# Optimization experiments

Hardware: AMD Instinct MI355X
Metric: run time of the kernel (lower is better)

Reference implementation:

```python
import jax, jax.numpy as jnp
import numpy as np

# Hypernetwork config (matches init_kwargs)
INP = 4096      # inp_size
MSK = 64        # mask_size
HID = 64        # node_hidden_size (target-net hidden)
OUT = 10        # out_size (target outputs)
L1, L2, L3 = 64, 256, 128  # hypernet trunk layers
B = 16384       # batch
WVEC = MSK * HID + HID + HID * OUT + OUT  # 4810 generated weights per sample


def _linear_params(key, fan_in, fan_out):
    # torch.nn.Linear default init: U(-1/sqrt(fan_in), 1/sqrt(fan_in))
    lim = 1.0 / np.sqrt(fan_in)
    kw, kb = jax.random.split(key)
    W = jax.random.uniform(kw, (fan_out, fan_in), minval=-lim, maxval=lim, dtype=jnp.float32)
    b = jax.random.uniform(kb, (fan_out,), minval=-lim, maxval=lim, dtype=jnp.float32)
    return W, b


def setup_inputs() -> dict:
    key = jax.random.key(0)
    ks = jax.random.split(key, 6)
    W1, b1 = _linear_params(ks[0], INP, L1)
    W2, b2 = _linear_params(ks[1], L1, L2)
    W3, b3 = _linear_params(ks[2], L2, L3)
    W4, b4 = _linear_params(ks[3], L3, WVEC)
    data = jax.random.normal(ks[4], (B, INP), dtype=jnp.float32)
    mask_idx = jnp.sort(jax.random.randint(ks[5], (B, MSK), 0, INP), axis=1)  # int indices of active features
    return dict(data=data, mask_idx=mask_idx,
                W1=W1, b1=b1, W2=W2, b2=b2, W3=W3, b3=b3, W4=W4, b4=b4)


def reference(data, mask_idx, W1, b1, W2, b2, W3, b3, W4, b4):
    b = data.shape[0]
    # Rebuild the float binary mask [B, INP] from indices (scatter ones)
    rows = jnp.arange(b)[:, None]
    mask = jnp.zeros((b, INP), dtype=data.dtype).at[rows, mask_idx].set(1.0)

    # craft_network: 4-layer MLP on the mask (dropout is identity in eval / for reference)
    h = jax.nn.relu(mask @ W1.T + b1)
    h = jax.nn.relu(h @ W2.T + b2)
    h = jax.nn.relu(h @ W3.T + b3)
    w = h @ W4.T + b4  # [B, WVEC] generated weights per sample

    # Split per-sample generated weights (same layout as InsertableNet)
    iw_end = MSK * HID
    ib_end = iw_end + HID
    ow_end = ib_end + HID * OUT
    inp_w = w[:, :iw_end].reshape(b, HID, MSK)       # [B, H, M]
    inp_b = w[:, iw_end:ib_end]                      # [B, H]
    out_w = w[:, ib_end:ow_end].reshape(b, OUT, HID) # [B, O, H]
    out_b = w[:, ow_end:]                            # [B, O]

    # Per-sample gather of masked features: data[i, mask[i]] -> [B, M]
    xm = jnp.take_along_axis(data, mask_idx, axis=1)

    # Batched tiny 2-layer MLP (replaces the per-sample Python loop)
    hid = jax.nn.relu(jnp.einsum('bhm,bm->bh', inp_w, xm) + inp_b)
    res = jnp.einsum('boh,bh->bo', out_w, hid) + out_b  # [B, OUT]
    return res
```

## Files before the change

### kernel.cpp

```cpp
#include <hip/hip_runtime.h>


typedef _Float16 f16;
typedef _Float16 f16x8 __attribute__((ext_vector_type(8)));
typedef _Float16 f16x4 __attribute__((ext_vector_type(4)));
typedef float    f32x4 __attribute__((ext_vector_type(4)));

#define NPAD 4864

#define BAR() do { asm volatile("s_waitcnt lgkmcnt(0)" ::: "memory"); \
                   __builtin_amdgcn_s_barrier();                      \
                   asm volatile("" ::: "memory"); } while (0)

__global__ __launch_bounds__(256) void k_prep(
    const float* __restrict__ W1, const float* __restrict__ W2,
    const float* __restrict__ W3, const float* __restrict__ W4,
    f16* __restrict__ W1Th, f16* __restrict__ W2h,
    f16* __restrict__ W3h, f16* __restrict__ W4s)
{
    const int bid = blockIdx.x;
    const int t = threadIdx.x;

    if (bid < 64) {
        __shared__ float tile[64][65];
        const int r4 = t >> 6, c0 = t & 63;
        #pragma unroll
        for (int rr = 0; rr < 16; ++rr) {
            const int i = rr * 4 + r4;
            tile[i][c0] = W1[(size_t)i * 4096 + bid * 64 + c0];
        }
        __syncthreads();
        #pragma unroll
        for (int rr = 0; rr < 16; ++rr) {
            const int jj = rr * 4 + r4;
            W1Th[(size_t)(bid * 64 + jj) * 64 + c0] = (f16)tile[c0][jj];
        }
        return;
    }

    const int tid = (bid - 64) * 256 + t;
    const int stride = (gridDim.x - 64) * 256;
    for (int e = tid; e < NPAD * 128; e += stride) {
        const int j    = e & 7;
        const int lane = (e >> 3) & 63;
        const int mt   = (e >> 9) & 3;
        const int kk   = (e >> 11) & 3;
        const int c    = e >> 13;
        const int lr = lane & 15, g = lane >> 4;
        const int row = 64 * c + 16 * mt + lr;
        const int col = 32 * kk + 8 * g + j;
        W4s[e] = (row < 4810) ? (f16)W4[(size_t)row * 128 + col] : (f16)0.f;
    }
    for (int e = tid; e < 256 * 64; e += stride)  W2h[e] = (f16)W2[e];
    for (int e = tid; e < 128 * 256; e += stride) W3h[e] = (f16)W3[e];
}

__global__ __launch_bounds__(512, 2) void k_main(
    const float* __restrict__ data, const int* __restrict__ midx,
    const f16* __restrict__ W1Th, const float* __restrict__ b1,
    const f16* __restrict__ W2h, const float* __restrict__ b2,
    const f16* __restrict__ W3h, const float* __restrict__ b3,
    const f16* __restrict__ W4s, const float* __restrict__ b4,
    float* __restrict__ out)
{
    __shared__ __align__(16) int   idx_s[64 * 64];
    __shared__ __align__(16) char  h1b[8192];
    __shared__ __align__(16) char  h2b[32768];
    __shared__ __align__(16) char  h3b[16384];
    __shared__ __align__(16) float xm_s[64 * 68];
    __shared__ __align__(16) float hid_s[64 * 68];
    __shared__ __align__(16) f16   w64_s[64 * 64];
    __shared__ __align__(16) float res_s[64 * 12];
    __shared__ __align__(16) float res_b[64 * 12];

    const int t = threadIdx.x, w = t >> 6, lane = t & 63;
    const int lr = lane & 15, g = lane >> 4;
    const int row0 = blockIdx.x * 64;
    const f32x4 zero = {0.f, 0.f, 0.f, 0.f};

    for (int e = t; e < 4096; e += 512)
        idx_s[e] = midx[(size_t)row0 * 64 + e];
    BAR();

    float xr[32];

    if (w >= 6) {
        const int base = (w - 6) * 32;
        #pragma unroll
        for (int k = 0; k < 32; ++k)
            xr[k] = data[(size_t)(row0 + base + k) * 4096 + idx_s[(base + k) * 64 + lane]];
        __builtin_amdgcn_sched_barrier(0);
    } else {
        const f32x4 b1v = *(const f32x4*)&b1[lr * 4];
        for (int sp = w; sp < 32; sp += 6) {
            const int s0 = 2 * sp, s1 = s0 + 1;
            f32x4 a0 = zero, a1 = zero;
            #pragma unroll
            for (int tt = 0; tt < 16; ++tt) {
                const int i = g * 16 + tt;
                const int c0 = idx_s[s0 * 64 + i];
                const int q0 = (i > 0) ? idx_s[s0 * 64 + i - 1] : -1;
                const int c1 = idx_s[s1 * 64 + i];
                const int q1 = (i > 0) ? idx_s[s1 * 64 + i - 1] : -1;
                const f16x4 w0 = *(const f16x4*)&W1Th[c0 * 64 + lr * 4];
                const f16x4 w1 = *(const f16x4*)&W1Th[c1 * 64 + lr * 4];
                #pragma unroll
                for (int q = 0; q < 4; ++q) {
                    a0[q] += (c0 != q0) ? (float)w0[q] : 0.f;
                    a1[q] += (c1 != q1) ? (float)w1[q] : 0.f;
                }
            }
            #pragma unroll
            for (int q = 0; q < 4; ++q) {
                a0[q] += __shfl_xor(a0[q], 16);
                a0[q] += __shfl_xor(a0[q], 32);
                a1[q] += __shfl_xor(a1[q], 16);
                a1[q] += __shfl_xor(a1[q], 32);
            }
            if (g == 0) {
                f16x4 h0, h1v;
                #pragma unroll
                for (int q = 0; q < 4; ++q) {
                    h0[q]  = (f16)fmaxf(a0[q] + b1v[q], 0.f);
                    h1v[q] = (f16)fmaxf(a1[q] + b1v[q], 0.f);
                }
                *(f16x4*)(h1b + ((s0 * 128 + lr * 8) ^ ((s0 & 7) << 4))) = h0;
                *(f16x4*)(h1b + ((s1 * 128 + lr * 8) ^ ((s1 & 7) << 4))) = h1v;
            }
        }
    }
    BAR();

    if (w < 6) {
        f16x8 bh[4][2];
        #pragma unroll
        for (int rt = 0; rt < 4; ++rt)
            #pragma unroll
            for (int kk = 0; kk < 2; ++kk) {
                const int s = 16 * rt + lr;
                bh[rt][kk] = *(const f16x8*)(h1b + ((s * 128 + (32 * kk + 8 * g) * 2) ^ ((s & 7) << 4)));
            }
        for (int nb = w; nb < 8; nb += 6) {
            const int n0 = 32 * nb;
            f16x8 a2[2][2];
            #pragma unroll
            for (int mt = 0; mt < 2; ++mt)
                #pragma unroll
                for (int kk = 0; kk < 2; ++kk)
                    a2[mt][kk] = *(const f16x8*)&W2h[(n0 + 16 * mt + lr) * 64 + 32 * kk + 8 * g];
            f32x4 acc2[2][4];
            #pragma unroll
            for (int mt = 0; mt < 2; ++mt)
                #pragma unroll
                for (int rt = 0; rt < 4; ++rt) {
                    acc2[mt][rt] = __builtin_amdgcn_mfma_f32_16x16x32_f16(a2[mt][0], bh[rt][0], zero, 0, 0, 0);
                    acc2[mt][rt] = __builtin_amdgcn_mfma_f32_16x16x32_f16(a2[mt][1], bh[rt][1], acc2[mt][rt], 0, 0, 0);
                }
            #pragma unroll
            for (int mt = 0; mt < 2; ++mt) {
                const f32x4 bv = *(const f32x4*)&b2[n0 + 16 * mt + 4 * g];
                #pragma unroll
                for (int rt = 0; rt < 4; ++rt) {
                    const int s = 16 * rt + lr;
                    f16x4 hv;
                    #pragma unroll
                    for (int q = 0; q < 4; ++q)
                        hv[q] = (f16)fmaxf(acc2[mt][rt][q] + bv[q], 0.f);
                    *(f16x4*)(h2b + ((s * 512 + (n0 + 16 * mt + 4 * g) * 2) ^ ((s & 7) << 4))) = hv;
                }
            }
        }
    }
    BAR();

    if (w < 6) {
        for (int nb = w; nb < 8; nb += 6) {
            const int n0 = 16 * nb;
            f32x4 acc3[4] = {zero, zero, zero, zero};
            #pragma unroll 2
            for (int kk = 0; kk < 8; ++kk) {
                const f16x8 a3 = *(const f16x8*)&W3h[(n0 + lr) * 256 + 32 * kk + 8 * g];
                #pragma unroll
                for (int rt = 0; rt < 4; ++rt) {
                    const int s = 16 * rt + lr;
                    const f16x8 bb = *(const f16x8*)(h2b + ((s * 512 + (32 * kk + 8 * g) * 2) ^ ((s & 7) << 4)));
                    acc3[rt] = __builtin_amdgcn_mfma_f32_16x16x32_f16(a3, bb, acc3[rt], 0, 0, 0);
                }
            }
            const f32x4 bv3 = *(const f32x4*)&b3[n0 + 4 * g];
            #pragma unroll
            for (int rt = 0; rt < 4; ++rt) {
                const int s = 16 * rt + lr;
                f16x4 hv;
                #pragma unroll
                for (int q = 0; q < 4; ++q)
                    hv[q] = (f16)fmaxf(acc3[rt][q] + bv3[q], 0.f);
                *(f16x4*)(h3b + ((s * 256 + (n0 + 4 * g) * 2) ^ ((s & 7) << 4))) = hv;
            }
        }
    }
    BAR();

    f16x8 bfrag[4][4];
    #pragma unroll
    for (int u = 0; u < 4; ++u)
        #pragma unroll
        for (int kk = 0; kk < 4; ++kk) {
            const int s = 16 * u + lr;
            bfrag[kk][u] = *(const f16x8*)(h3b + ((s * 256 + (32 * kk + 8 * g) * 2) ^ ((s & 7) << 4)));
        }
    if (w >= 6) {
        const int base = (w - 6) * 32;
        #pragma unroll
        for (int k = 0; k < 32; ++k)
            xm_s[(base + k) * 68 + lane] = xr[k];
    }
    BAR();

    f16x4 xmr[4][4];
    #pragma unroll
    for (int mt = 0; mt < 4; ++mt)
        #pragma unroll
        for (int u = 0; u < 4; ++u) {
            const f32x4 xv = *(const f32x4*)&xm_s[(16 * u + lr) * 68 + 16 * mt + 4 * g];
            f16x4 xh;
            #pragma unroll
            for (int q = 0; q < 4; ++q) xh[q] = (f16)xv[q];
            xmr[mt][u] = xh;
        }

    const char* W4b = (const char*)W4s;
    const int afoff = lane * 16;

#define LDAF(dst, c, kk) { const char* cb_ = W4b + (size_t)(c) * 16384 + (kk) * 4096 + afoff; \
    dst[0] = *(const f16x8*)(cb_);        dst[1] = *(const f16x8*)(cb_ + 1024); \
    dst[2] = *(const f16x8*)(cb_ + 2048); dst[3] = *(const f16x8*)(cb_ + 3072); }

#define MFMA16(af, kk) { \
    _Pragma("unroll") for (int mt = 0; mt < 4; ++mt) \
    _Pragma("unroll") for (int u = 0; u < 4; ++u) \
        acc[mt][u] = __builtin_amdgcn_mfma_f32_16x16x32_f16(af[mt], bfrag[kk][u], acc[mt][u], 0, 0, 0); }

    for (int c = w; c < 65; c += 8) {
        f16x8 afA[4], afB[4];
        LDAF(afA, c, 0)
        LDAF(afB, c, 1)
        f32x4 acc[4][4];
        #pragma unroll
        for (int mt = 0; mt < 4; ++mt)
            #pragma unroll
            for (int u = 0; u < 4; ++u)
                acc[mt][u] = __builtin_amdgcn_mfma_f32_16x16x32_f16(afA[mt], bfrag[0][u], zero, 0, 0, 0);
        LDAF(afA, c, 2)
        MFMA16(afB, 1)
        LDAF(afB, c, 3)
        MFMA16(afA, 2)
        MFMA16(afB, 3)

        f32x4 bv[4];
        #pragma unroll
        for (int mt = 0; mt < 4; ++mt)
            bv[mt] = *(const f32x4*)&b4[64 * c + 16 * mt + 4 * g];

        if (c < 64) {
            #pragma unroll
            for (int u = 0; u < 4; ++u) {
                float sum = 0.f;
                #pragma unroll
                for (int mt = 0; mt < 4; ++mt)
                    #pragma unroll
                    for (int q = 0; q < 4; ++q)
                        sum += (acc[mt][u][q] + bv[mt][q]) * (float)xmr[mt][u][q];
                sum += __shfl_xor(sum, 16);
                sum += __shfl_xor(sum, 32);
                if (g == 0) hid_s[(16 * u + lr) * 68 + c] = sum;
            }
        } else {
            #pragma unroll
            for (int u = 0; u < 4; ++u)
                #pragma unroll
                for (int mt = 0; mt < 4; ++mt) {
                    f16x4 wv;
                    #pragma unroll
                    for (int q = 0; q < 4; ++q)
                        wv[q] = (f16)(acc[mt][u][q] + bv[mt][q]);
                    *(f16x4*)&w64_s[(16 * u + lr) * 64 + 16 * mt + 4 * g] = wv;
                }
        }
    }
    BAR();

    f16x4 hidr[4][4];
    #pragma unroll
    for (int mt = 0; mt < 4; ++mt)
        #pragma unroll
        for (int u = 0; u < 4; ++u) {
            const int s = 16 * u + lr;
            f16x4 xh;
            #pragma unroll
            for (int q = 0; q < 4; ++q) {
                const int h = 16 * mt + 4 * g + q;
                xh[q] = (f16)fmaxf(hid_s[s * 68 + h] + (float)w64_s[s * 64 + h], 0.f);
            }
            hidr[mt][u] = xh;
        }

    auto do_out = [&](int c) {
        f32x4 bv[4];
        #pragma unroll
        for (int mt = 0; mt < 4; ++mt)
            bv[mt] = *(const f32x4*)&b4[64 * c + 16 * mt + 4 * g];
        f16x8 afA[4], afB[4];
        LDAF(afA, c, 0)
        LDAF(afB, c, 1)
        f32x4 acc[4][4];
        #pragma unroll
        for (int mt = 0; mt < 4; ++mt)
            #pragma unroll
            for (int u = 0; u < 4; ++u)
                acc[mt][u] = __builtin_amdgcn_mfma_f32_16x16x32_f16(afA[mt], bfrag[0][u], zero, 0, 0, 0);
        LDAF(afA, c, 2)
        MFMA16(afB, 1)
        LDAF(afB, c, 3)
        MFMA16(afA, 2)
        MFMA16(afB, 3)
        #pragma unroll
        for (int u = 0; u < 4; ++u) {
            float sum = 0.f;
            #pragma unroll
            for (int mt = 0; mt < 4; ++mt)
                #pragma unroll
                for (int q = 0; q < 4; ++q)
                    sum += (acc[mt][u][q] + bv[mt][q]) * (float)hidr[mt][u][q];
            sum += __shfl_xor(sum, 16);
            sum += __shfl_xor(sum, 32);
            if (g == 0) res_s[(16 * u + lr) * 12 + (c - 65)] = sum;
        }
    };
    do_out(65 + w);
    if (w < 2) do_out(73 + w);

    if (w == 2) {
        f32x4 accb[4] = {zero, zero, zero, zero};
        #pragma unroll
        for (int kk = 0; kk < 4; ++kk) {
            const f16x8 af = *(const f16x8*)(W4b + (size_t)75 * 16384 + kk * 4096 + afoff);
            #pragma unroll
            for (int u = 0; u < 4; ++u)
                accb[u] = __builtin_amdgcn_mfma_f32_16x16x32_f16(af, bfrag[kk][u], accb[u], 0, 0, 0);
        }
        #pragma unroll
        for (int u = 0; u < 4; ++u)
            #pragma unroll
            for (int q = 0; q < 4; ++q) {
                const int o = 4 * g + q;
                if (o < 10)
                    res_b[(16 * u + lr) * 12 + o] = accb[u][q] + b4[4800 + o];
            }
    }
    BAR();

    for (int e = t; e < 640; e += 512)
        out[(size_t)row0 * 10 + e] =
            res_s[(e / 10) * 12 + (e % 10)] + res_b[(e / 10) * 12 + (e % 10)];
#undef LDAF
#undef MFMA16
}

extern "C" void kernel_launch(void* const* d_in, const int* in_sizes, int n_in,
                              void* d_out, int out_size, void* d_ws, size_t ws_size,
                              hipStream_t stream)
{
    const float* data = (const float*)d_in[0];
    const int*   midx = (const int*)d_in[1];
    const float* W1   = (const float*)d_in[2];
    const float* b1   = (const float*)d_in[3];
    const float* W2   = (const float*)d_in[4];
    const float* b2   = (const float*)d_in[5];
    const float* W3   = (const float*)d_in[6];
    const float* b3   = (const float*)d_in[7];
    const float* W4   = (const float*)d_in[8];
    const float* b4   = (const float*)d_in[9];
    float* out = (float*)d_out;

    f16* W1Th = (f16*)d_ws;
    f16* W4s  = W1Th + (size_t)4096 * 64;
    f16* W2h  = W4s + (size_t)NPAD * 128;
    f16* W3h  = W2h + 256 * 64;

    k_prep<<<512, 256, 0, stream>>>(W1, W2, W3, W4, W1Th, W2h, W3h, W4s);
    k_main<<<256, 512, 0, stream>>>(data, midx, W1Th, b1, W2h, b2, W3h, b3,
                                    W4s, b4, out);
}
```

Measured before the change: 75.26 us.

## Split W4 GEMM into two row halves and stagger data gathers across phases

```diff
diff --git a/kernel.cpp b/kernel.cpp
--- a/kernel.cpp
+++ b/kernel.cpp
@@ -84,13 +84,12 @@
 
     float xr[32];
 
-    if (w >= 6) {
-        const int base = (w - 6) * 32;
+    if (w == 6) {
         #pragma unroll
         for (int k = 0; k < 32; ++k)
-            xr[k] = data[(size_t)(row0 + base + k) * 4096 + idx_s[(base + k) * 64 + lane]];
+            xr[k] = data[(size_t)(row0 + k) * 4096 + idx_s[k * 64 + lane]];
         __builtin_amdgcn_sched_barrier(0);
-    } else {
+    } else if (w < 6) {
         const f32x4 b1v = *(const f32x4*)&b1[lr * 4];
         for (int sp = w; sp < 32; sp += 6) {
             const int s0 = 2 * sp, s1 = s0 + 1;
@@ -131,7 +130,12 @@
     }
     BAR();
 
-    if (w < 6) {
+    if (w == 7) {
+        #pragma unroll
+        for (int k = 0; k < 32; ++k)
+            xr[k] = data[(size_t)(row0 + 32 + k) * 4096 + idx_s[(32 + k) * 64 + lane]];
+        __builtin_amdgcn_sched_barrier(0);
+    } else if (w < 6) {
         f16x8 bh[4][2];
         #pragma unroll
         for (int rt = 0; rt < 4; ++rt)
@@ -201,170 +205,169 @@
     }
     BAR();
 
-    f16x8 bfrag[4][4];
-    #pragma unroll
-    for (int u = 0; u < 4; ++u)
-        #pragma unroll
-        for (int kk = 0; kk < 4; ++kk) {
-            const int s = 16 * u + lr;
-            bfrag[kk][u] = *(const f16x8*)(h3b + ((s * 256 + (32 * kk + 8 * g) * 2) ^ ((s & 7) << 4)));
-        }
-    if (w >= 6) {
-        const int base = (w - 6) * 32;
+    if (w == 6) {
         #pragma unroll
         for (int k = 0; k < 32; ++k)
-            xm_s[(base + k) * 68 + lane] = xr[k];
-    }
-    BAR();
-
-    f16x4 xmr[4][4];
-    #pragma unroll
-    for (int mt = 0; mt < 4; ++mt)
-        #pragma unroll
-        for (int u = 0; u < 4; ++u) {
-            const f32x4 xv = *(const f32x4*)&xm_s[(16 * u + lr) * 68 + 16 * mt + 4 * g];
-            f16x4 xh;
-            #pragma unroll
-            for (int q = 0; q < 4; ++q) xh[q] = (f16)xv[q];
-            xmr[mt][u] = xh;
-        }
+            xm_s[k * 68 + lane] = xr[k];
+    }
+    BAR();
 
     const char* W4b = (const char*)W4s;
     const int afoff = lane * 16;
 
-#define LDAF(dst, c, kk) { const char* cb_ = W4b + (size_t)(c) * 16384 + (kk) * 4096 + afoff; \
-    dst[0] = *(const f16x8*)(cb_);        dst[1] = *(const f16x8*)(cb_ + 1024); \
-    dst[2] = *(const f16x8*)(cb_ + 2048); dst[3] = *(const f16x8*)(cb_ + 3072); }
-
-#define MFMA16(af, kk) { \
-    _Pragma("unroll") for (int mt = 0; mt < 4; ++mt) \
-    _Pragma("unroll") for (int u = 0; u < 4; ++u) \
-        acc[mt][u] = __builtin_amdgcn_mfma_f32_16x16x32_f16(af[mt], bfrag[kk][u], acc[mt][u], 0, 0, 0); }
-
-    for (int c = w; c < 65; c += 8) {
-        f16x8 afA[4], afB[4];
-        LDAF(afA, c, 0)
-        LDAF(afB, c, 1)
-        f32x4 acc[4][4];
+    auto gemm_chunk = [&](int c, const f16x8 bf[4][2], f32x4 acc[4][2]) {
         #pragma unroll
         for (int mt = 0; mt < 4; ++mt)
             #pragma unroll
-            for (int u = 0; u < 4; ++u)
-                acc[mt][u] = __builtin_amdgcn_mfma_f32_16x16x32_f16(afA[mt], bfrag[0][u], zero, 0, 0, 0);
-        LDAF(afA, c, 2)
-        MFMA16(afB, 1)
-        LDAF(afB, c, 3)
-        MFMA16(afA, 2)
-        MFMA16(afB, 3)
-
-        f32x4 bv[4];
+            for (int u2 = 0; u2 < 2; ++u2) acc[mt][u2] = zero;
+        #pragma unroll
+        for (int kk = 0; kk < 4; ++kk) {
+            f16x8 af[4];
+            const char* cb_ = W4b + (size_t)c * 16384 + kk * 4096 + afoff;
+            af[0] = *(const f16x8*)(cb_);
+            af[1] = *(const f16x8*)(cb_ + 1024);
+            af[2] = *(const f16x8*)(cb_ + 2048);
+            af[3] = *(const f16x8*)(cb_ + 3072);
+            #pragma unroll
+            for (int mt = 0; mt < 4; ++mt)
+                #pragma unroll
+                for (int u2 = 0; u2 < 2; ++u2)
+                    acc[mt][u2] = __builtin_amdgcn_mfma_f32_16x16x32_f16(af[mt], bf[kk][u2], acc[mt][u2], 0, 0, 0);
+        }
+    };
+    auto load_bfrag = [&](f16x8 bf[4][2], int h) {
+        #pragma unroll
+        for (int u2 = 0; u2 < 2; ++u2)
+            #pragma unroll
+            for (int kk = 0; kk < 4; ++kk) {
+                const int s = 32 * h + 16 * u2 + lr;
+                bf[kk][u2] = *(const f16x8*)(h3b + ((s * 256 + (32 * kk + 8 * g) * 2) ^ ((s & 7) << 4)));
+            }
+    };
+    auto do_inp = [&](int h, int nw) {
+        f16x8 bf[4][2];
+        load_bfrag(bf, h);
+        f16x4 xmr[4][2];
         #pragma unroll
         for (int mt = 0; mt < 4; ++mt)
-            bv[mt] = *(const f32x4*)&b4[64 * c + 16 * mt + 4 * g];
-
-        if (c < 64) {
-            #pragma unroll
-            for (int u = 0; u < 4; ++u) {
-                float sum = 0.f;
+            #pragma unroll
+            for (int u2 = 0; u2 < 2; ++u2) {
+                const f32x4 xv = *(const f32x4*)&xm_s[(32 * h + 16 * u2 + lr) * 68 + 16 * mt + 4 * g];
+                f16x4 xh;
+                #pragma unroll
+                for (int q = 0; q < 4; ++q) xh[q] = (f16)xv[q];
+                xmr[mt][u2] = xh;
+            }
+        for (int c = w; c < 65; c += nw) {
+            f32x4 acc[4][2];
+            gemm_chunk(c, bf, acc);
+            f32x4 bv[4];
+            #pragma unroll
+            for (int mt = 0; mt < 4; ++mt)
+                bv[mt] = *(const f32x4*)&b4[64 * c + 16 * mt + 4 * g];
+            if (c < 64) {
+                #pragma unroll
+                for (int u2 = 0; u2 < 2; ++u2) {
+                    float sum = 0.f;
+                    #pragma unroll
+                    for (int mt = 0; mt < 4; ++mt)
+                        #pragma unroll
+                        for (int q = 0; q < 4; ++q)
+                            sum += (acc[mt][u2][q] + bv[mt][q]) * (float)xmr[mt][u2][q];
+                    sum += __shfl_xor(sum, 16);
+                    sum += __shfl_xor(sum, 32);
+                    if (g == 0) hid_s[(32 * h + 16 * u2 + lr) * 68 + c] = sum;
+                }
+            } else {
+                #pragma unroll
+                for (int u2 = 0; u2 < 2; ++u2)
+                    #pragma unroll
+                    for (int mt = 0; mt < 4; ++mt) {
+                        f16x4 wv;
+                        #pragma unroll
+                        for (int q = 0; q < 4; ++q)
+                            wv[q] = (f16)(acc[mt][u2][q] + bv[mt][q]);
+                        *(f16x4*)&w64_s[(32 * h + 16 * u2 + lr) * 64 + 16 * mt + 4 * g] = wv;
+                    }
+            }
+        }
+    };
+
+    if (w < 7) {
+        do_inp(0, 7);
+    } else {
+        #pragma unroll
+        for (int k = 0; k < 32; ++k)
+            xm_s[(32 + k) * 68 + lane] = xr[k];
+    }
+    BAR();
+
+    do_inp(1, 8);
+    BAR();
+
+    {
+        const int h = (w >= 4), wid = w & 3;
+        f16x8 bf[4][2];
+        load_bfrag(bf, h);
+        f16x4 hidr[4][2];
+        #pragma unroll
+        for (int mt = 0; mt < 4; ++mt)
+            #pragma unroll
+            for (int u2 = 0; u2 < 2; ++u2) {
+                const int s = 32 * h + 16 * u2 + lr;
+                f16x4 xh;
+                #pragma unroll
+                for (int q = 0; q < 4; ++q) {
+                    const int hh = 16 * mt + 4 * g + q;
+                    xh[q] = (f16)fmaxf(hid_s[s * 68 + hh] + (float)w64_s[s * 64 + hh], 0.f);
+                }
+                hidr[mt][u2] = xh;
+            }
+        for (int c = 65 + wid; c <= 75; c += 4) {
+            if (c < 75) {
+                f32x4 acc[4][2];
+                gemm_chunk(c, bf, acc);
+                f32x4 bv[4];
                 #pragma unroll
                 for (int mt = 0; mt < 4; ++mt)
-                    #pragma unroll
-                    for (int q = 0; q < 4; ++q)
-                        sum += (acc[mt][u][q] + bv[mt][q]) * (float)xmr[mt][u][q];
-                sum += __shfl_xor(sum, 16);
-                sum += __shfl_xor(sum, 32);
-                if (g == 0) hid_s[(16 * u + lr) * 68 + c] = sum;
-            }
-        } else {
-            #pragma unroll
-            for (int u = 0; u < 4; ++u)
-                #pragma unroll
-                for (int mt = 0; mt < 4; ++mt) {
-                    f16x4 wv;
-                    #pragma unroll
-                    for (int q = 0; q < 4; ++q)
-                        wv[q] = (f16)(acc[mt][u][q] + bv[mt][q]);
-                    *(f16x4*)&w64_s[(16 * u + lr) * 64 + 16 * mt + 4 * g] = wv;
-                }
-        }
-    }
-    BAR();
-
-    f16x4 hidr[4][4];
-    #pragma unroll
-    for (int mt = 0; mt < 4; ++mt)
-        #pragma unroll
-        for (int u = 0; u < 4; ++u) {
-            const int s = 16 * u + lr;
-            f16x4 xh;
-            #pragma unroll
-            for (int q = 0; q < 4; ++q) {
-                const int h = 16 * mt + 4 * g + q;
-                xh[q] = (f16)fmaxf(hid_s[s * 68 + h] + (float)w64_s[s * 64 + h], 0.f);
-            }
-            hidr[mt][u] = xh;
-        }
-
-    auto do_out = [&](int c) {
-        f32x4 bv[4];
-        #pragma unroll
-        for (int mt = 0; mt < 4; ++mt)
-            bv[mt] = *(const f32x4*)&b4[64 * c + 16 * mt + 4 * g];
-        f16x8 afA[4], afB[4];
-        LDAF(afA, c, 0)
-        LDAF(afB, c, 1)
-        f32x4 acc[4][4];
-        #pragma unroll
-        for (int mt = 0; mt < 4; ++mt)
-            #pragma unroll
-            for (int u = 0; u < 4; ++u)
-                acc[mt][u] = __builtin_amdgcn_mfma_f32_16x16x32_f16(afA[mt], bfrag[0][u], zero, 0, 0, 0);
-        LDAF(afA, c, 2)
-        MFMA16(afB, 1)
-        LDAF(afB, c, 3)
-        MFMA16(afA, 2)
-        MFMA16(afB, 3)
-        #pragma unroll
-        for (int u = 0; u < 4; ++u) {
-            float sum = 0.f;
-            #pragma unroll
-            for (int mt = 0; mt < 4; ++mt)
-                #pragma unroll
-                for (int q = 0; q < 4; ++q)
-                    sum += (acc[mt][u][q] + bv[mt][q]) * (float)hidr[mt][u][q];
-            sum += __shfl_xor(sum, 16);
-            sum += __shfl_xor(sum, 32);
-            if (g == 0) res_s[(16 * u + lr) * 12 + (c - 65)] = sum;
-        }
-    };
-    do_out(65 + w);
-    if (w < 2) do_out(73 + w);
-
-    if (w == 2) {
-        f32x4 accb[4] = {zero, zero, zero, zero};
-        #pragma unroll
-        for (int kk = 0; kk < 4; ++kk) {
-            const f16x8 af = *(const f16x8*)(W4b + (size_t)75 * 16384 + kk * 4096 + afoff);
-            #pragma unroll
-            for (int u = 0; u < 4; ++u)
-                accb[u] = __builtin_amdgcn_mfma_f32_16x16x32_f16(af, bfrag[kk][u], accb[u], 0, 0, 0);
-        }
-        #pragma unroll
-        for (int u = 0; u < 4; ++u)
-            #pragma unroll
-            for (int q = 0; q < 4; ++q) {
-                const int o = 4 * g + q;
-                if (o < 10)
-                    res_b[(16 * u + lr) * 12 + o] = accb[u][q] + b4[4800 + o];
-            }
+                    bv[mt] = *(const f32x4*)&b4[64 * c + 16 * mt + 4 * g];
+                #pragma unroll
+                for (int u2 = 0; u2 < 2; ++u2) {
+                    float sum = 0.f;
+                    #pragma unroll
+                    for (int mt = 0; mt < 4; ++mt)
+                        #pragma unroll
+                        for (int q = 0; q < 4; ++q)
+                            sum += (acc[mt][u2][q] + bv[mt][q]) * (float)hidr[mt][u2][q];
+                    sum += __shfl_xor(sum, 16);
+                    sum += __shfl_xor(sum, 32);
+                    if (g == 0) res_s[(32 * h + 16 * u2 + lr) * 12 + (c - 65)] = sum;
+                }
+            } else {
+                f32x4 accb[2] = {zero, zero};
+                #pragma unroll
+                for (int kk = 0; kk < 4; ++kk) {
+                    const f16x8 af = *(const f16x8*)(W4b + (size_t)75 * 16384 + kk * 4096 + afoff);
+                    #pragma unroll
+                    for (int u2 = 0; u2 < 2; ++u2)
+                        accb[u2] = __builtin_amdgcn_mfma_f32_16x16x32_f16(af, bf[kk][u2], accb[u2], 0, 0, 0);
+                }
+                #pragma unroll
+                for (int u2 = 0; u2 < 2; ++u2)
+                    #pragma unroll
+                    for (int q = 0; q < 4; ++q) {
+                        const int o = 4 * g + q;
+                        if (o < 10)
+                            res_b[(32 * h + 16 * u2 + lr) * 12 + o] = accb[u2][q] + b4[4800 + o];
+                    }
+            }
+        }
     }
     BAR();
 
     for (int e = t; e < 640; e += 512)
         out[(size_t)row0 * 10 + e] =
             res_s[(e / 10) * 12 + (e % 10)] + res_b[(e / 10) * 12 + (e % 10)];
-#undef LDAF
-#undef MFMA16
 }
 
 extern "C" void kernel_launch(void* const* d_in, const int* in_sizes, int n_in,
```

Measured after the change: 84.30 us. 1.12x slower.

## Halve rows per block to 32 and double grid to 512 blocks

Applied to the files above, without the earlier changes.

```diff
diff --git a/kernel.cpp b/kernel.cpp
--- a/kernel.cpp
+++ b/kernel.cpp
@@ -55,7 +55,7 @@
     for (int e = tid; e < 128 * 256; e += stride) W3h[e] = (f16)W3[e];
 }
 
-__global__ __launch_bounds__(512, 2) void k_main(
+__global__ __launch_bounds__(512, 4) void k_main(
     const float* __restrict__ data, const int* __restrict__ midx,
     const f16* __restrict__ W1Th, const float* __restrict__ b1,
     const f16* __restrict__ W2h, const float* __restrict__ b2,
@@ -63,36 +63,35 @@
     const f16* __restrict__ W4s, const float* __restrict__ b4,
     float* __restrict__ out)
 {
-    __shared__ __align__(16) int   idx_s[64 * 64];
-    __shared__ __align__(16) char  h1b[8192];
-    __shared__ __align__(16) char  h2b[32768];
-    __shared__ __align__(16) char  h3b[16384];
-    __shared__ __align__(16) float xm_s[64 * 68];
-    __shared__ __align__(16) float hid_s[64 * 68];
-    __shared__ __align__(16) f16   w64_s[64 * 64];
-    __shared__ __align__(16) float res_s[64 * 12];
-    __shared__ __align__(16) float res_b[64 * 12];
+    __shared__ __align__(16) int   idx_s[32 * 64];
+    __shared__ __align__(16) char  h1b[4096];
+    __shared__ __align__(16) char  h2b[16384];
+    __shared__ __align__(16) char  h3b[8192];
+    __shared__ __align__(16) float xm_s[32 * 68];
+    __shared__ __align__(16) float hid_s[32 * 68];
+    __shared__ __align__(16) f16   w64_s[32 * 64];
+    __shared__ __align__(16) float res_s[32 * 12];
+    __shared__ __align__(16) float res_b[32 * 12];
 
     const int t = threadIdx.x, w = t >> 6, lane = t & 63;
     const int lr = lane & 15, g = lane >> 4;
-    const int row0 = blockIdx.x * 64;
+    const int row0 = blockIdx.x * 32;
     const f32x4 zero = {0.f, 0.f, 0.f, 0.f};
 
-    for (int e = t; e < 4096; e += 512)
+    for (int e = t; e < 2048; e += 512)
         idx_s[e] = midx[(size_t)row0 * 64 + e];
     BAR();
 
     float xr[32];
 
-    if (w >= 6) {
-        const int base = (w - 6) * 32;
+    if (w == 7) {
         #pragma unroll
         for (int k = 0; k < 32; ++k)
-            xr[k] = data[(size_t)(row0 + base + k) * 4096 + idx_s[(base + k) * 64 + lane]];
+            xr[k] = data[(size_t)(row0 + k) * 4096 + idx_s[k * 64 + lane]];
         __builtin_amdgcn_sched_barrier(0);
     } else {
         const f32x4 b1v = *(const f32x4*)&b1[lr * 4];
-        for (int sp = w; sp < 32; sp += 6) {
+        for (int sp = w; sp < 16; sp += 7) {
             const int s0 = 2 * sp, s1 = s0 + 1;
             f32x4 a0 = zero, a1 = zero;
             #pragma unroll
@@ -131,16 +130,16 @@
     }
     BAR();
 
-    if (w < 6) {
-        f16x8 bh[4][2];
-        #pragma unroll
-        for (int rt = 0; rt < 4; ++rt)
+    if (w < 7) {
+        f16x8 bh[2][2];
+        #pragma unroll
+        for (int rt = 0; rt < 2; ++rt)
             #pragma unroll
             for (int kk = 0; kk < 2; ++kk) {
                 const int s = 16 * rt + lr;
                 bh[rt][kk] = *(const f16x8*)(h1b + ((s * 128 + (32 * kk + 8 * g) * 2) ^ ((s & 7) << 4)));
             }
-        for (int nb = w; nb < 8; nb += 6) {
+        for (int nb = w; nb < 8; nb += 7) {
             const int n0 = 32 * nb;
             f16x8 a2[2][2];
             #pragma unroll
@@ -148,11 +147,11 @@
                 #pragma unroll
                 for (int kk = 0; kk < 2; ++kk)
                     a2[mt][kk] = *(const f16x8*)&W2h[(n0 + 16 * mt + lr) * 64 + 32 * kk + 8 * g];
-            f32x4 acc2[2][4];
+            f32x4 acc2[2][2];
             #pragma unroll
             for (int mt = 0; mt < 2; ++mt)
                 #pragma unroll
-                for (int rt = 0; rt < 4; ++rt) {
+                for (int rt = 0; rt < 2; ++rt) {
                     acc2[mt][rt] = __builtin_amdgcn_mfma_f32_16x16x32_f16(a2[mt][0], bh[rt][0], zero, 0, 0, 0);
                     acc2[mt][rt] = __builtin_amdgcn_mfma_f32_16x16x32_f16(a2[mt][1], bh[rt][1], acc2[mt][rt], 0, 0, 0);
                 }
@@ -160,7 +159,7 @@
             for (int mt = 0; mt < 2; ++mt) {
                 const f32x4 bv = *(const f32x4*)&b2[n0 + 16 * mt + 4 * g];
                 #pragma unroll
-                for (int rt = 0; rt < 4; ++rt) {
+                for (int rt = 0; rt < 2; ++rt) {
                     const int s = 16 * rt + lr;
                     f16x4 hv;
                     #pragma unroll
@@ -173,15 +172,15 @@
     }
     BAR();
 
-    if (w < 6) {
-        for (int nb = w; nb < 8; nb += 6) {
+    if (w < 7) {
+        for (int nb = w; nb < 8; nb += 7) {
             const int n0 = 16 * nb;
-            f32x4 acc3[4] = {zero, zero, zero, zero};
+            f32x4 acc3[2] = {zero, zero};
             #pragma unroll 2
             for (int kk = 0; kk < 8; ++kk) {
                 const f16x8 a3 = *(const f16x8*)&W3h[(n0 + lr) * 256 + 32 * kk + 8 * g];
                 #pragma unroll
-                for (int rt = 0; rt < 4; ++rt) {
+                for (int rt = 0; rt < 2; ++rt) {
                     const int s = 16 * rt + lr;
                     const f16x8 bb = *(const f16x8*)(h2b + ((s * 512 + (32 * kk + 8 * g) * 2) ^ ((s & 7) << 4)));
                     acc3[rt] = __builtin_amdgcn_mfma_f32_16x16x32_f16(a3, bb, acc3[rt], 0, 0, 0);
@@ -189,7 +188,7 @@
             }
             const f32x4 bv3 = *(const f32x4*)&b3[n0 + 4 * g];
             #pragma unroll
-            for (int rt = 0; rt < 4; ++rt) {
+            for (int rt = 0; rt < 2; ++rt) {
                 const int s = 16 * rt + lr;
                 f16x4 hv;
                 #pragma unroll
@@ -201,27 +200,26 @@
     }
     BAR();
 
-    f16x8 bfrag[4][4];
+    f16x8 bfrag[4][2];
     #pragma unroll
-    for (int u = 0; u < 4; ++u)
+    for (int u = 0; u < 2; ++u)
         #pragma unroll
         for (int kk = 0; kk < 4; ++kk) {
             const int s = 16 * u + lr;
             bfrag[kk][u] = *(const f16x8*)(h3b + ((s * 256 + (32 * kk + 8 * g) * 2) ^ ((s & 7) << 4)));
         }
-    if (w >= 6) {
-        const int base = (w - 6) * 32;
+    if (w == 7) {
         #pragma unroll
         for (int k = 0; k < 32; ++k)
-            xm_s[(base + k) * 68 + lane] = xr[k];
-    }
-    BAR();
-
-    f16x4 xmr[4][4];
+            xm_s[k * 68 + lane] = xr[k];
+    }
+    BAR();
+
+    f16x4 xmr[4][2];
     #pragma unroll
     for (int mt = 0; mt < 4; ++mt)
         #pragma unroll
-        for (int u = 0; u < 4; ++u) {
+        for (int u = 0; u < 2; ++u) {
             const f32x4 xv = *(const f32x4*)&xm_s[(16 * u + lr) * 68 + 16 * mt + 4 * g];
             f16x4 xh;
             #pragma unroll
@@ -236,26 +234,23 @@
     dst[0] = *(const f16x8*)(cb_);        dst[1] = *(const f16x8*)(cb_ + 1024); \
     dst[2] = *(const f16x8*)(cb_ + 2048); dst[3] = *(const f16x8*)(cb_ + 3072); }
 
-#define MFMA16(af, kk) { \
+#define MFMA8(af, kk) { \
     _Pragma("unroll") for (int mt = 0; mt < 4; ++mt) \
-    _Pragma("unroll") for (int u = 0; u < 4; ++u) \
+    _Pragma("unroll") for (int u = 0; u < 2; ++u) \
         acc[mt][u] = __builtin_amdgcn_mfma_f32_16x16x32_f16(af[mt], bfrag[kk][u], acc[mt][u], 0, 0, 0); }
 
     for (int c = w; c < 65; c += 8) {
-        f16x8 afA[4], afB[4];
-        LDAF(afA, c, 0)
-        LDAF(afB, c, 1)
-        f32x4 acc[4][4];
+        f32x4 acc[4][2];
         #pragma unroll
         for (int mt = 0; mt < 4; ++mt)
             #pragma unroll
-            for (int u = 0; u < 4; ++u)
-                acc[mt][u] = __builtin_amdgcn_mfma_f32_16x16x32_f16(afA[mt], bfrag[0][u], zero, 0, 0, 0);
-        LDAF(afA, c, 2)
-        MFMA16(afB, 1)
-        LDAF(afB, c, 3)
-        MFMA16(afA, 2)
-        MFMA16(afB, 3)
+            for (int u = 0; u < 2; ++u) acc[mt][u] = zero;
+        #pragma unroll
+        for (int kk = 0; kk < 4; ++kk) {
+            f16x8 af[4];
+            LDAF(af, c, kk)
+            MFMA8(af, kk)
+        }
 
         f32x4 bv[4];
         #pragma unroll
@@ -264,7 +259,7 @@
 
         if (c < 64) {
             #pragma unroll
-            for (int u = 0; u < 4; ++u) {
+            for (int u = 0; u < 2; ++u) {
                 float sum = 0.f;
                 #pragma unroll
                 for (int mt = 0; mt < 4; ++mt)
@@ -277,7 +272,7 @@
             }
         } else {
             #pragma unroll
-            for (int u = 0; u < 4; ++u)
+            for (int u = 0; u < 2; ++u)
                 #pragma unroll
                 for (int mt = 0; mt < 4; ++mt) {
                     f16x4 wv;
@@ -290,11 +285,11 @@
     }
     BAR();
 
-    f16x4 hidr[4][4];
+    f16x4 hidr[4][2];
     #pragma unroll
     for (int mt = 0; mt < 4; ++mt)
         #pragma unroll
-        for (int u = 0; u < 4; ++u) {
+        for (int u = 0; u < 2; ++u) {
             const int s = 16 * u + lr;
             f16x4 xh;
             #pragma unroll
@@ -310,22 +305,19 @@
         #pragma unroll
         for (int mt = 0; mt < 4; ++mt)
             bv[mt] = *(const f32x4*)&b4[64 * c + 16 * mt + 4 * g];
-        f16x8 afA[4], afB[4];
-        LDAF(afA, c, 0)
-        LDAF(afB, c, 1)
-        f32x4 acc[4][4];
+        f32x4 acc[4][2];
         #pragma unroll
         for (int mt = 0; mt < 4; ++mt)
             #pragma unroll
-            for (int u = 0; u < 4; ++u)
-                acc[mt][u] = __builtin_amdgcn_mfma_f32_16x16x32_f16(afA[mt], bfrag[0][u], zero, 0, 0, 0);
-        LDAF(afA, c, 2)
-        MFMA16(afB, 1)
-        LDAF(afB, c, 3)
-        MFMA16(afA, 2)
-        MFMA16(afB, 3)
-        #pragma unroll
-        for (int u = 0; u < 4; ++u) {
+            for (int u = 0; u < 2; ++u) acc[mt][u] = zero;
+        #pragma unroll
+        for (int kk = 0; kk < 4; ++kk) {
+            f16x8 af[4];
+            LDAF(af, c, kk)
+            MFMA8(af, kk)
+        }
+        #pragma unroll
+        for (int u = 0; u < 2; ++u) {
             float sum = 0.f;
             #pragma unroll
             for (int mt = 0; mt < 4; ++mt)
@@ -341,16 +333,16 @@
     if (w < 2) do_out(73 + w);
 
     if (w == 2) {
-        f32x4 accb[4] = {zero, zero, zero, zero};
+        f32x4 accb[2] = {zero, zero};
         #pragma unroll
         for (int kk = 0; kk < 4; ++kk) {
             const f16x8 af = *(const f16x8*)(W4b + (size_t)75 * 16384 + kk * 4096 + afoff);
             #pragma unroll
-            for (int u = 0; u < 4; ++u)
+            for (int u = 0; u < 2; ++u)
                 accb[u] = __builtin_amdgcn_mfma_f32_16x16x32_f16(af, bfrag[kk][u], accb[u], 0, 0, 0);
         }
         #pragma unroll
-        for (int u = 0; u < 4; ++u)
+        for (int u = 0; u < 2; ++u)
             #pragma unroll
             for (int q = 0; q < 4; ++q) {
                 const int o = 4 * g + q;
@@ -360,11 +352,11 @@
     }
     BAR();
 
-    for (int e = t; e < 640; e += 512)
+    for (int e = t; e < 320; e += 512)
         out[(size_t)row0 * 10 + e] =
             res_s[(e / 10) * 12 + (e % 10)] + res_b[(e / 10) * 12 + (e % 10)];
 #undef LDAF
-#undef MFMA16
+#undef MFMA8
 }
 
 extern "C" void kernel_launch(void* const* d_in, const int* in_sizes, int n_in,
@@ -389,6 +381,6 @@
     f16* W3h  = W2h + 256 * 64;
 
     k_prep<<<512, 256, 0, stream>>>(W1, W2, W3, W4, W1Th, W2h, W3h, W4s);
-    k_main<<<256, 512, 0, stream>>>(data, midx, W1Th, b1, W2h, b2, W3h, b3,
+    k_main<<<512, 512, 0, stream>>>(data, midx, W1Th, b1, W2h, b2, W3h, b3,
                                     W4s, b4, out);
 }
```

Measured after the change: 75.89 us. No clear change (+0.8%).
